# Kernel optimization log

Hardware: AMD Instinct MI355X
Metric: run time of the kernel (lower is better)

Reference implementation:

```python
import jax, jax.numpy as jnp
import numpy as np

MIN_NORM = 1e-5
PROJ_EPS = 4e-3  # geoopt poincare ball boundary eps


def expmap0(u, c):
    # exponential map at origin of the Poincare ball: tanh(sqrt(c)||u||) * u / (sqrt(c)||u||)
    sqrt_c = jnp.sqrt(c)
    u_norm = jnp.maximum(jnp.linalg.norm(u, axis=-1, keepdims=True), MIN_NORM)
    return jnp.tanh(sqrt_c * u_norm) * u / (sqrt_c * u_norm)


def project(x, c):
    # clip points to stay strictly inside the ball of radius (1-eps)/sqrt(c)
    norm = jnp.maximum(jnp.linalg.norm(x, axis=-1, keepdims=True), MIN_NORM)
    maxnorm = (1.0 - PROJ_EPS) / jnp.sqrt(c)
    return jnp.where(norm > maxnorm, x / norm * maxnorm, x)


def setup_inputs() -> dict:
    key = jax.random.key(0)
    k1, k2, k3 = jax.random.split(key, 3)
    n, m, d = 4096, 4096, 1024
    query = jax.random.normal(k1, (n, d), dtype=jnp.float32)
    context = jax.random.normal(k2, (m, d), dtype=jnp.float32)
    W = jax.random.normal(k3, (d, d), dtype=jnp.float32) / np.sqrt(d)  # linear_in weight
    c = jnp.ones((1,), dtype=jnp.float32)  # curvature parameter
    return {"query": query, "context": context, "W": W, "c": c}


def reference(query, context, W, c):
    n, d = query.shape
    q = project(expmap0(query, c), c)
    ctx = project(expmap0(context, c), c)
    q = q @ W.T                      # linear_in (no bias), [n, d]
    scores = q @ ctx.T               # [n, m]
    attn = jax.nn.softmax(scores / d, axis=1)
    attn = project(expmap0(attn, c), c)
    return attn
```

## Files before the change

### kernel.cpp

```cpp
#include <hip/hip_runtime.h>
#include <cstdint>


typedef unsigned short ushort_t;
typedef __bf16 bf16x8 __attribute__((ext_vector_type(8)));
typedef float f32x4 __attribute__((ext_vector_type(4)));
typedef float f32x16 __attribute__((ext_vector_type(16)));
typedef int i32x4 __attribute__((ext_vector_type(4)));
typedef int i32x8 __attribute__((ext_vector_type(8)));

__device__ __forceinline__ unsigned short f32_to_bf16(float f) {
  unsigned int u = __float_as_uint(f);
  u = (u + 0x7fffu + ((u >> 16) & 1u)) >> 16;
  return (unsigned short)u;
}

__device__ __forceinline__ unsigned char f32_to_fp8(float f) {
  int p = __builtin_amdgcn_cvt_pk_fp8_f32(f, f, 0, false);
  return (unsigned char)(p & 0xFF);
}

__device__ __forceinline__ void async_copy16(const void* g, void* s) {
  __builtin_amdgcn_global_load_lds(
      (const __attribute__((address_space(1))) void*)g,
      (__attribute__((address_space(3))) void*)s, 16, 0, 0);
}

__global__ void prep_q(const float* __restrict__ q, const float* __restrict__ W,
                       ushort_t* __restrict__ qn, ushort_t* __restrict__ Wb,
                       const float* __restrict__ cptr, int n) {
  const int b = blockIdx.x;
  const int tid = threadIdx.x;

  if (b >= n) {
    int i = (b - n) * 256 + tid;
    float4 v = reinterpret_cast<const float4*>(W)[i];
    reinterpret_cast<ushort4*>(Wb)[i] =
        make_ushort4(f32_to_bf16(v.x), f32_to_bf16(v.y), f32_to_bf16(v.z), f32_to_bf16(v.w));
    return;
  }

  const int lane = tid & 63, w = tid >> 6;
  __shared__ float red[4];
  const float* x = q + (size_t)b * 1024;
  ushort_t* out = qn + (size_t)b * 1024;

  float4 v = reinterpret_cast<const float4*>(x)[tid];
  float ss = v.x * v.x + v.y * v.y + v.z * v.z + v.w * v.w;
#pragma unroll
  for (int o = 32; o; o >>= 1) ss += __shfl_down(ss, o, 64);
  if (lane == 0) red[w] = ss;
  __syncthreads();
  ss = red[0] + red[1] + red[2] + red[3];

  const float c = *cptr;
  const float sqrtc = sqrtf(c);
  const float norm = fmaxf(sqrtf(ss), 1e-5f);
  const float t = tanhf(sqrtc * norm) / (sqrtc * norm);
  const float en = fmaxf(t * norm, 1e-5f);
  const float maxn = (1.0f - 4e-3f) / sqrtc;
  const float s = t * (en > maxn ? maxn / en : 1.0f);

  reinterpret_cast<ushort4*>(out)[tid] =
      make_ushort4(f32_to_bf16(v.x * s), f32_to_bf16(v.y * s),
                   f32_to_bf16(v.z * s), f32_to_bf16(v.w * s));
}

__global__ void qw_ctx(const ushort_t* __restrict__ A,
                       const ushort_t* __restrict__ B,
                       unsigned char* __restrict__ Cb,
                       const float* __restrict__ ctx, unsigned char* __restrict__ cn,
                       const float* __restrict__ cptr, int K, int N, int nGemm) {
  __shared__ __align__(16) ushort_t As[128 * 32];
  __shared__ __align__(16) ushort_t Bs[64 * 32];

  const int tid = threadIdx.x;

  if (blockIdx.x >= nGemm) {
    const int r = blockIdx.x - nGemm;
    const int lane = tid & 63, wv = tid >> 6;
    float* red = reinterpret_cast<float*>(As);
    const float* x = ctx + (size_t)r * 1024;
    unsigned char* out = cn + (size_t)r * 1024;

    float4 v = reinterpret_cast<const float4*>(x)[tid];
    float ss = v.x * v.x + v.y * v.y + v.z * v.z + v.w * v.w;
#pragma unroll
    for (int o = 32; o; o >>= 1) ss += __shfl_down(ss, o, 64);
    if (lane == 0) red[wv] = ss;
    __syncthreads();
    ss = red[0] + red[1] + red[2] + red[3];

    const float c = *cptr;
    const float sqrtc = sqrtf(c);
    const float norm = fmaxf(sqrtf(ss), 1e-5f);
    const float t = tanhf(sqrtc * norm) / (sqrtc * norm);
    const float en = fmaxf(t * norm, 1e-5f);
    const float maxn = (1.0f - 4e-3f) / sqrtc;
    const float s = t * (en > maxn ? maxn / en : 1.0f);

    int lo = __builtin_amdgcn_cvt_pk_fp8_f32(v.x * s, v.y * s, 0, false);
    int pk = __builtin_amdgcn_cvt_pk_fp8_f32(v.z * s, v.w * s, lo, true);
    reinterpret_cast<int*>(out)[tid] = pk;
    return;
  }

  const int gx = blockIdx.x & 31;
  const int gy = blockIdx.x >> 5;
  const int w = tid >> 6;
  const int lane = tid & 63;
  const int lane15 = lane & 15;
  const int quad = lane >> 4;
  const int wr = w >> 1, wc = w & 1;

  const size_t rowBase = (size_t)gx * 128;
  const size_t colBase = (size_t)gy * 64;

  const int srow = lane >> 2;
  const int scolE = (lane & 3) * 8;
  const ushort_t* Ag = A + (rowBase + (size_t)(w * 32 + srow)) * K + scolE;
  const ushort_t* Bg = B + (colBase + (size_t)(w * 16 + srow)) * K + scolE;
  ushort_t* AsD = &As[w * 1024];
  ushort_t* BsD = &Bs[w * 512];

  f32x4 acc[4][2];
#pragma unroll
  for (int i = 0; i < 4; ++i)
#pragma unroll
    for (int j = 0; j < 2; ++j) acc[i][j] = f32x4{0.f, 0.f, 0.f, 0.f};

  for (int k0 = 0; k0 < K; k0 += 32) {
    async_copy16(Ag + k0, AsD);
    async_copy16(Ag + (size_t)16 * K + k0, AsD + 512);
    async_copy16(Bg + k0, BsD);
    __syncthreads();

    bf16x8 af[4], bv[2];
#pragma unroll
    for (int i = 0; i < 4; ++i)
      af[i] = *reinterpret_cast<const bf16x8*>(&As[(wr * 64 + i * 16 + lane15) * 32 + quad * 8]);
#pragma unroll
    for (int j = 0; j < 2; ++j)
      bv[j] = *reinterpret_cast<const bf16x8*>(&Bs[(wc * 32 + j * 16 + lane15) * 32 + quad * 8]);
#pragma unroll
    for (int i = 0; i < 4; ++i)
#pragma unroll
      for (int j = 0; j < 2; ++j)
        acc[i][j] = __builtin_amdgcn_mfma_f32_16x16x32_bf16(af[i], bv[j], acc[i][j], 0, 0, 0);
    __syncthreads();
  }

#pragma unroll
  for (int i = 0; i < 4; ++i)
#pragma unroll
    for (int j = 0; j < 2; ++j)
#pragma unroll
      for (int r = 0; r < 4; ++r) {
        size_t row = rowBase + (size_t)(wr * 64 + i * 16 + quad * 4 + r);
        size_t col = colBase + (size_t)(wc * 32 + j * 16 + lane15);
        Cb[row * N + col] = f32_to_fp8(acc[i][j][r]);
      }
}


#define MFMA8(a, b, c) \
  __builtin_amdgcn_mfma_scale_f32_32x32x64_f8f6f4(a, b, c, 0, 0, 0, 0x7F7F7F7F, 0, 0x7F7F7F7F)

__device__ __forceinline__ i32x8 ld_frag(const unsigned char* p, int off) {
  i32x4 lo = *reinterpret_cast<const i32x4*>(p + off);
  i32x4 hi = *reinterpret_cast<const i32x4*>(p + (off ^ 16));
  return __builtin_shufflevector(lo, hi, 0, 1, 2, 3, 4, 5, 6, 7);
}

#define SUBTILE8(BUF, DOSTAGE, K0S)                                              \
  do {                                                                           \
    const unsigned char* As_ = &As[BUF][0];                                      \
    const unsigned char* Bs_ = &Bs[BUF][0];                                      \
    i32x8 af0 = ld_frag(As_, aO);                                                \
    i32x8 af1 = ld_frag(As_, aO + 2048);                                         \
    i32x8 bf0 = ld_frag(Bs_, bO);                                                \
    i32x8 bf1 = ld_frag(Bs_, bO + 2048);                                         \
    __builtin_amdgcn_s_setprio(1);                                               \
    acc[0][0] = MFMA8(af0, bf0, acc[0][0]);                                      \
    acc[0][1] = MFMA8(af0, bf1, acc[0][1]);                                      \
    acc[1][0] = MFMA8(af1, bf0, acc[1][0]);                                      \
    acc[1][1] = MFMA8(af1, bf1, acc[1][1]);                                      \
    __builtin_amdgcn_s_setprio(0);                                               \
    i32x8 af2 = ld_frag(As_, aO + 2 * 2048);                                     \
    i32x8 af3 = ld_frag(As_, aO + 3 * 2048);                                     \
    __builtin_amdgcn_s_setprio(1);                                               \
    acc[2][0] = MFMA8(af2, bf0, acc[2][0]);                                      \
    acc[2][1] = MFMA8(af2, bf1, acc[2][1]);                                      \
    __builtin_amdgcn_s_setprio(0);                                               \
    asm volatile("s_waitcnt lgkmcnt(0)" ::: "memory"); \
    __builtin_amdgcn_sched_barrier(0);                                           \
    __builtin_amdgcn_s_barrier();                         \
    if (DOSTAGE) {                             \
      async_copy16(Ag + (size_t)(K0S), &As[BUF][w * 1024]);                      \
      async_copy16(Ag + (size_t)128 * K + (K0S), &As[BUF][8192 + w * 1024]);     \
    }                                                                            \
    __builtin_amdgcn_s_setprio(1);                                               \
    acc[3][0] = MFMA8(af3, bf0, acc[3][0]);                                      \
    __builtin_amdgcn_s_setprio(0);                                               \
    if (DOSTAGE) {                             \
      async_copy16(Bg + (size_t)(K0S), &Bs[BUF][w * 1024]);                      \
      async_copy16(Bg + (size_t)128 * K + (K0S), &Bs[BUF][8192 + w * 1024]);     \
    }                                                                            \
    __builtin_amdgcn_s_setprio(1);                                               \
    acc[3][1] = MFMA8(af3, bf1, acc[3][1]);                                      \
    __builtin_amdgcn_s_setprio(0);                                               \
  } while (0)

__global__ __launch_bounds__(512) void gemm_sc(const unsigned char* __restrict__ A,
                                               const unsigned char* __restrict__ B,
                                               ushort_t* __restrict__ Sb, int K, int N) {
  __shared__ __align__(16) unsigned char As[2][16384];
  __shared__ __align__(16) unsigned char Bs[2][16384];

  const int tid = threadIdx.x;
  const int w = tid >> 6;
  const int lane = tid & 63;
  const int l31 = lane & 31;
  const int wm = w >> 2;
  const int wn = w & 3;

  const size_t rowBase = (size_t)blockIdx.x * 256;
  const size_t colBase = (size_t)blockIdx.y * 256;

  const int srcC = ((tid & 3) ^ ((tid >> 3) & 3)) * 16;
  const unsigned char* Ag = A + (rowBase + (size_t)(tid >> 2)) * K + srcC;
  const unsigned char* Bg = B + (colBase + (size_t)(tid >> 2)) * K + srcC;

  const int x2 = (lane >> 1) & 3;
  const int kc0 = (lane >> 5) * 2;
  const int chunkOff = (kc0 ^ x2) * 16;
  const int aO = (wm * 128 + l31) * 64 + chunkOff;
  const int bO = (wn * 64 + l31) * 64 + chunkOff;

  f32x16 acc[4][2];
#pragma unroll
  for (int mi = 0; mi < 4; ++mi)
#pragma unroll
    for (int ni = 0; ni < 2; ++ni)
#pragma unroll
      for (int r = 0; r < 16; ++r) acc[mi][ni][r] = 0.f;

  async_copy16(Ag, &As[0][w * 1024]);
  async_copy16(Ag + (size_t)128 * K, &As[0][8192 + w * 1024]);
  async_copy16(Bg, &Bs[0][w * 1024]);
  async_copy16(Bg + (size_t)128 * K, &Bs[0][8192 + w * 1024]);
  async_copy16(Ag + 64, &As[1][w * 1024]);
  async_copy16(Ag + (size_t)128 * K + 64, &As[1][8192 + w * 1024]);
  async_copy16(Bg + 64, &Bs[1][w * 1024]);
  async_copy16(Bg + (size_t)128 * K + 64, &Bs[1][8192 + w * 1024]);
  asm volatile("s_waitcnt vmcnt(4)" ::: "memory");
  __builtin_amdgcn_s_barrier();

  for (int i = 0; i < 8; ++i) {
    const bool st = (i < 7);
    const int k0s = i * 128 + 128;
    SUBTILE8(0, st, k0s);
    if (st) { asm volatile("s_waitcnt vmcnt(4)" ::: "memory"); }
    else    { asm volatile("s_waitcnt vmcnt(0)" ::: "memory"); }
    __builtin_amdgcn_s_barrier();
    SUBTILE8(1, st, k0s + 64);
    if (st) {
      asm volatile("s_waitcnt vmcnt(4)" ::: "memory");
      __builtin_amdgcn_s_barrier();
    }
  }

  const int rq = lane >> 5;
#pragma unroll
  for (int mi = 0; mi < 4; ++mi)
#pragma unroll
    for (int ni = 0; ni < 2; ++ni)
#pragma unroll
      for (int r = 0; r < 16; ++r) {
        size_t row = rowBase + (size_t)(wm * 128 + mi * 32 + (r & 3) + 8 * (r >> 2) + 4 * rq);
        size_t col = colBase + (size_t)(wn * 64 + ni * 32 + l31);
        Sb[row * N + col] = f32_to_bf16(acc[mi][ni][r]);
      }
}

__global__ void softmax_hyp(const ushort_t* __restrict__ S, float* __restrict__ out,
                            const float* __restrict__ cptr, float invd) {
  const int tid = threadIdx.x;
  const int lane = tid & 63, w = tid >> 6;
  __shared__ float redS[4], redQ[4];
  const ushort_t* rp = S + (size_t)blockIdx.x * 4096;
  float* op = out + (size_t)blockIdx.x * 4096;

  float e[16];
  float sum = 0.f, sq = 0.f;
#pragma unroll
  for (int i = 0; i < 2; ++i) {
    uint4 u = reinterpret_cast<const uint4*>(rp)[i * 256 + tid];
    unsigned int uw[4] = {u.x, u.y, u.z, u.w};
#pragma unroll
    for (int k = 0; k < 4; ++k) {
      float lo = __uint_as_float(uw[k] << 16);
      float hi = __uint_as_float(uw[k] & 0xffff0000u);
      float elo = __expf(lo * invd);
      float ehi = __expf(hi * invd);
      e[i * 8 + k * 2] = elo;
      e[i * 8 + k * 2 + 1] = ehi;
      sum += elo + ehi;
      sq += elo * elo + ehi * ehi;
    }
  }
#pragma unroll
  for (int o = 32; o; o >>= 1) {
    sum += __shfl_down(sum, o, 64);
    sq += __shfl_down(sq, o, 64);
  }
  if (lane == 0) { redS[w] = sum; redQ[w] = sq; }
  __syncthreads();
  sum = redS[0] + redS[1] + redS[2] + redS[3];
  sq = redQ[0] + redQ[1] + redQ[2] + redQ[3];

  const float c = *cptr;
  const float sqrtc = sqrtf(c);
  const float anorm = sqrtf(sq) / sum;
  const float an = fmaxf(anorm, 1e-5f);
  const float t = tanhf(sqrtc * an) / (sqrtc * an);
  const float pn = fmaxf(t * anorm, 1e-5f);
  const float maxn = (1.0f - 4e-3f) / sqrtc;
  const float g = t * (pn > maxn ? maxn / pn : 1.0f) / sum;

#pragma unroll
  for (int i = 0; i < 2; ++i)
#pragma unroll
    for (int k = 0; k < 2; ++k) {
      float4 o = make_float4(e[i * 8 + k * 4] * g, e[i * 8 + k * 4 + 1] * g,
                             e[i * 8 + k * 4 + 2] * g, e[i * 8 + k * 4 + 3] * g);
      reinterpret_cast<float4*>(op)[(i * 256 + tid) * 2 + k] = o;
    }
}

extern "C" void kernel_launch(void* const* d_in, const int* in_sizes, int n_in,
                              void* d_out, int out_size, void* d_ws, size_t ws_size,
                              hipStream_t stream) {
  const float* query = (const float*)d_in[0];
  const float* context = (const float*)d_in[1];
  const float* W = (const float*)d_in[2];
  const float* cptr = (const float*)d_in[3];

  const int d = 1024;
  const int n = in_sizes[0] / d;
  const int m = in_sizes[1] / d;

  unsigned char* cn8 = (unsigned char*)d_ws;
  unsigned char* qw8 = cn8 + (size_t)m * d;
  ushort_t* qn = (ushort_t*)(qw8 + (size_t)n * d);
  ushort_t* Wb = qn + (size_t)n * d;
  ushort_t* scoresB = qn;
  float* attn = (float*)d_out;

  const int nGemm = (n / 128) * (d / 64);

  prep_q<<<n + d * d / 1024, 256, 0, stream>>>(query, W, qn, Wb, cptr, n);
  qw_ctx<<<nGemm + m, 256, 0, stream>>>(qn, Wb, qw8, context, cn8, cptr, d, d, nGemm);
  gemm_sc<<<dim3(n / 256, m / 256), 512, 0, stream>>>(qw8, cn8, scoresB, d, m);
  softmax_hyp<<<n, 256, 0, stream>>>(scoresB, attn, cptr, 1.0f / (float)d);
}
```

Measured before the change: 150.9 us.

## Convert q@W^T projection GEMM from bf16 to fp8 MFMA with swizzled LDS

The normalized query and the weight matrix are now stored as fp8 instead of bf16. The first GEMM uses the 32x32x64 fp8 scaled MFMA with K-step 64 and an XOR-swizzled LDS layout in place of bf16 16x16x32 MFMAs. This halves the bytes moved for the q and W staging and doubles MFMA throughput per instruction. The cost is lower precision in the projected queries and W, which could hurt accuracy. The workspace layout changes so scores no longer alias qn, which increases workspace use.

Measured after the change: 140.7 us. 6.8% less time.

```diff
diff --git a/kernel.cpp b/kernel.cpp
--- a/kernel.cpp
+++ b/kernel.cpp
@@ -20,14 +20,28 @@
   return (unsigned char)(p & 0xFF);
 }
 
+__device__ __forceinline__ int pack4_fp8(float a, float b, float c, float d) {
+  int lo = __builtin_amdgcn_cvt_pk_fp8_f32(a, b, 0, false);
+  return __builtin_amdgcn_cvt_pk_fp8_f32(c, d, lo, true);
+}
+
 __device__ __forceinline__ void async_copy16(const void* g, void* s) {
   __builtin_amdgcn_global_load_lds(
       (const __attribute__((address_space(1))) void*)g,
       (__attribute__((address_space(3))) void*)s, 16, 0, 0);
 }
 
+#define MFMA8(a, b, c) \
+  __builtin_amdgcn_mfma_scale_f32_32x32x64_f8f6f4(a, b, c, 0, 0, 0, 0x7F7F7F7F, 0, 0x7F7F7F7F)
+
+__device__ __forceinline__ i32x8 ld_frag(const unsigned char* p, int off) {
+  i32x4 lo = *reinterpret_cast<const i32x4*>(p + off);
+  i32x4 hi = *reinterpret_cast<const i32x4*>(p + (off ^ 16));
+  return __builtin_shufflevector(lo, hi, 0, 1, 2, 3, 4, 5, 6, 7);
+}
+
 __global__ void prep_q(const float* __restrict__ q, const float* __restrict__ W,
-                       ushort_t* __restrict__ qn, ushort_t* __restrict__ Wb,
+                       unsigned char* __restrict__ qn8, unsigned char* __restrict__ Wb8,
                        const float* __restrict__ cptr, int n) {
   const int b = blockIdx.x;
   const int tid = threadIdx.x;
@@ -35,15 +49,14 @@
   if (b >= n) {
     int i = (b - n) * 256 + tid;
     float4 v = reinterpret_cast<const float4*>(W)[i];
-    reinterpret_cast<ushort4*>(Wb)[i] =
-        make_ushort4(f32_to_bf16(v.x), f32_to_bf16(v.y), f32_to_bf16(v.z), f32_to_bf16(v.w));
+    reinterpret_cast<int*>(Wb8)[i] = pack4_fp8(v.x, v.y, v.z, v.w);
     return;
   }
 
   const int lane = tid & 63, w = tid >> 6;
   __shared__ float red[4];
   const float* x = q + (size_t)b * 1024;
-  ushort_t* out = qn + (size_t)b * 1024;
+  unsigned char* out = qn8 + (size_t)b * 1024;
 
   float4 v = reinterpret_cast<const float4*>(x)[tid];
   float ss = v.x * v.x + v.y * v.y + v.z * v.z + v.w * v.w;
@@ -61,18 +74,16 @@
   const float maxn = (1.0f - 4e-3f) / sqrtc;
   const float s = t * (en > maxn ? maxn / en : 1.0f);
 
-  reinterpret_cast<ushort4*>(out)[tid] =
-      make_ushort4(f32_to_bf16(v.x * s), f32_to_bf16(v.y * s),
-                   f32_to_bf16(v.z * s), f32_to_bf16(v.w * s));
-}
-
-__global__ void qw_ctx(const ushort_t* __restrict__ A,
-                       const ushort_t* __restrict__ B,
+  reinterpret_cast<int*>(out)[tid] = pack4_fp8(v.x * s, v.y * s, v.z * s, v.w * s);
+}
+
+__global__ void qw_ctx(const unsigned char* __restrict__ A,
+                       const unsigned char* __restrict__ B,
                        unsigned char* __restrict__ Cb,
                        const float* __restrict__ ctx, unsigned char* __restrict__ cn,
                        const float* __restrict__ cptr, int K, int N, int nGemm) {
-  __shared__ __align__(16) ushort_t As[128 * 32];
-  __shared__ __align__(16) ushort_t Bs[64 * 32];
+  __shared__ __align__(16) unsigned char As[128 * 64];
+  __shared__ __align__(16) unsigned char Bs[64 * 64];
 
   const int tid = threadIdx.x;
 
@@ -99,9 +110,7 @@
     const float maxn = (1.0f - 4e-3f) / sqrtc;
     const float s = t * (en > maxn ? maxn / en : 1.0f);
 
-    int lo = __builtin_amdgcn_cvt_pk_fp8_f32(v.x * s, v.y * s, 0, false);
-    int pk = __builtin_amdgcn_cvt_pk_fp8_f32(v.z * s, v.w * s, lo, true);
-    reinterpret_cast<int*>(out)[tid] = pk;
+    reinterpret_cast<int*>(out)[tid] = pack4_fp8(v.x * s, v.y * s, v.z * s, v.w * s);
     return;
   }
 
@@ -109,68 +118,52 @@
   const int gy = blockIdx.x >> 5;
   const int w = tid >> 6;
   const int lane = tid & 63;
-  const int lane15 = lane & 15;
-  const int quad = lane >> 4;
+  const int l31 = lane & 31;
   const int wr = w >> 1, wc = w & 1;
 
   const size_t rowBase = (size_t)gx * 128;
   const size_t colBase = (size_t)gy * 64;
 
-  const int srow = lane >> 2;
-  const int scolE = (lane & 3) * 8;
-  const ushort_t* Ag = A + (rowBase + (size_t)(w * 32 + srow)) * K + scolE;
-  const ushort_t* Bg = B + (colBase + (size_t)(w * 16 + srow)) * K + scolE;
-  ushort_t* AsD = &As[w * 1024];
-  ushort_t* BsD = &Bs[w * 512];
-
-  f32x4 acc[4][2];
-#pragma unroll
-  for (int i = 0; i < 4; ++i)
-#pragma unroll
-    for (int j = 0; j < 2; ++j) acc[i][j] = f32x4{0.f, 0.f, 0.f, 0.f};
-
-  for (int k0 = 0; k0 < K; k0 += 32) {
-    async_copy16(Ag + k0, AsD);
-    async_copy16(Ag + (size_t)16 * K + k0, AsD + 512);
-    async_copy16(Bg + k0, BsD);
+  const int srcC = ((tid & 3) ^ ((tid >> 3) & 3)) * 16;
+  const unsigned char* Ag = A + (rowBase + (size_t)(tid >> 2)) * K + srcC;
+  const unsigned char* Bg = B + (colBase + (size_t)(tid >> 2)) * K + srcC;
+
+  const int x2 = (lane >> 1) & 3;
+  const int chunkOff = (((lane >> 5) * 2) ^ x2) * 16;
+  const int aO = (wr * 64 + l31) * 64 + chunkOff;
+  const int bO = (wc * 32 + l31) * 64 + chunkOff;
+
+  f32x16 acc[2];
+#pragma unroll
+  for (int mi = 0; mi < 2; ++mi)
+#pragma unroll
+    for (int r = 0; r < 16; ++r) acc[mi][r] = 0.f;
+
+  for (int k0 = 0; k0 < K; k0 += 64) {
+    async_copy16(Ag + k0, &As[w * 1024]);
+    async_copy16(Ag + (size_t)64 * K + k0, &As[4096 + w * 1024]);
+    async_copy16(Bg + k0, &Bs[w * 1024]);
     __syncthreads();
 
-    bf16x8 af[4], bv[2];
-#pragma unroll
-    for (int i = 0; i < 4; ++i)
-      af[i] = *reinterpret_cast<const bf16x8*>(&As[(wr * 64 + i * 16 + lane15) * 32 + quad * 8]);
-#pragma unroll
-    for (int j = 0; j < 2; ++j)
-      bv[j] = *reinterpret_cast<const bf16x8*>(&Bs[(wc * 32 + j * 16 + lane15) * 32 + quad * 8]);
-#pragma unroll
-    for (int i = 0; i < 4; ++i)
-#pragma unroll
-      for (int j = 0; j < 2; ++j)
-        acc[i][j] = __builtin_amdgcn_mfma_f32_16x16x32_bf16(af[i], bv[j], acc[i][j], 0, 0, 0);
+    i32x8 a0 = ld_frag(As, aO);
+    i32x8 a1 = ld_frag(As, aO + 2048);
+    i32x8 b0 = ld_frag(Bs, bO);
+    acc[0] = MFMA8(a0, b0, acc[0]);
+    acc[1] = MFMA8(a1, b0, acc[1]);
     __syncthreads();
   }
 
-#pragma unroll
-  for (int i = 0; i < 4; ++i)
-#pragma unroll
-    for (int j = 0; j < 2; ++j)
-#pragma unroll
-      for (int r = 0; r < 4; ++r) {
-        size_t row = rowBase + (size_t)(wr * 64 + i * 16 + quad * 4 + r);
-        size_t col = colBase + (size_t)(wc * 32 + j * 16 + lane15);
-        Cb[row * N + col] = f32_to_fp8(acc[i][j][r]);
-      }
-}
-
-
-#define MFMA8(a, b, c) \
-  __builtin_amdgcn_mfma_scale_f32_32x32x64_f8f6f4(a, b, c, 0, 0, 0, 0x7F7F7F7F, 0, 0x7F7F7F7F)
-
-__device__ __forceinline__ i32x8 ld_frag(const unsigned char* p, int off) {
-  i32x4 lo = *reinterpret_cast<const i32x4*>(p + off);
-  i32x4 hi = *reinterpret_cast<const i32x4*>(p + (off ^ 16));
-  return __builtin_shufflevector(lo, hi, 0, 1, 2, 3, 4, 5, 6, 7);
-}
+  const int rq = lane >> 5;
+#pragma unroll
+  for (int mi = 0; mi < 2; ++mi)
+#pragma unroll
+    for (int r = 0; r < 16; ++r) {
+      size_t row = rowBase + (size_t)(wr * 64 + mi * 32 + (r & 3) + 8 * (r >> 2) + 4 * rq);
+      size_t col = colBase + (size_t)(wc * 32 + l31);
+      Cb[row * N + col] = f32_to_fp8(acc[mi][r]);
+    }
+}
+
 
 #define SUBTILE8(BUF, DOSTAGE, K0S)                                              \
   do {                                                                           \
@@ -352,15 +345,15 @@
 
   unsigned char* cn8 = (unsigned char*)d_ws;
   unsigned char* qw8 = cn8 + (size_t)m * d;
-  ushort_t* qn = (ushort_t*)(qw8 + (size_t)n * d);
-  ushort_t* Wb = qn + (size_t)n * d;
-  ushort_t* scoresB = qn;
+  unsigned char* qn8 = qw8 + (size_t)n * d;
+  unsigned char* Wb8 = qn8 + (size_t)n * d;
+  ushort_t* scoresB = (ushort_t*)(Wb8 + (size_t)d * d);
   float* attn = (float*)d_out;
 
   const int nGemm = (n / 128) * (d / 64);
 
-  prep_q<<<n + d * d / 1024, 256, 0, stream>>>(query, W, qn, Wb, cptr, n);
-  qw_ctx<<<nGemm + m, 256, 0, stream>>>(qn, Wb, qw8, context, cn8, cptr, d, d, nGemm);
+  prep_q<<<n + d * d / 1024, 256, 0, stream>>>(query, W, qn8, Wb8, cptr, n);
+  qw_ctx<<<nGemm + m, 256, 0, stream>>>(qn8, Wb8, qw8, context, cn8, cptr, d, d, nGemm);
   gemm_sc<<<dim3(n / 256, m / 256), 512, 0, stream>>>(qw8, cn8, scoresB, d, m);
   softmax_hyp<<<n, 256, 0, stream>>>(scoresB, attn, cptr, 1.0f / (float)d);
 }
```
